# Kernel optimization log

Hardware: AMD Instinct MI355X
Metric: run time of the kernel (lower is better)

## Reference

```python
import jax, jax.numpy as jnp
import numpy as np

B, C, H, W = 8, 512, 128, 128
WS = 8

def _proj(x, w, b):
    # 1x1 conv == channel GEMM: (B,C,H,W) x (Cout,Cin) -> (B,Cout,H,W)
    return jnp.einsum('bchw,oc->bohw', x, w) + b[None, :, None, None]

def _split_windows(x):
    # (B,C,H,W) -> (B*nH*nW, ws*ws, C)
    b, c, h, w = x.shape
    x = x.reshape(b, c, h // WS, WS, w // WS, WS)
    x = x.transpose(0, 2, 4, 3, 5, 1)
    return x.reshape(-1, WS * WS, c)

def _merge_windows(x, b, c, h, w):
    # (B*nH*nW, ws*ws, C) -> (B,C,H,W)
    x = x.reshape(b, h // WS, w // WS, WS, WS, c)
    x = x.transpose(0, 5, 1, 3, 2, 4)
    return x.reshape(b, c, h, w)

def setup_inputs() -> dict:
    key = jax.random.key(0)
    ks = jax.random.split(key, 9)
    s = 1.0 / np.sqrt(C)
    return {
        'x': jax.random.normal(ks[0], (B, C, H, W), jnp.float32),
        'wq': jax.random.normal(ks[1], (C, C), jnp.float32) * s,
        'bq': jnp.zeros((C,), jnp.float32),
        'wk': jax.random.normal(ks[2], (C, C), jnp.float32) * s,
        'bk': jnp.zeros((C,), jnp.float32),
        'wv': jax.random.normal(ks[3], (C, C), jnp.float32) * s,
        'bv': jnp.zeros((C,), jnp.float32),
        'wo': jax.random.normal(ks[4], (C, C), jnp.float32) * s,
        'bo': jnp.zeros((C,), jnp.float32),
    }

def reference(x, wq, bq, wk, bk, wv, bv, wo, bo):
    b, c, h, w = x.shape
    q = _split_windows(_proj(x, wq, bq))  # (nWin, ws*ws, C)
    k = _split_windows(_proj(x, wk, bk))
    v = _split_windows(_proj(x, wv, bv))
    attn = jnp.einsum('nqc,nkc->nqk', q, k) / jnp.sqrt(jnp.asarray(c, x.dtype))
    attn = jax.nn.softmax(attn, axis=-1)
    out = jnp.einsum('nqk,nkc->nqc', attn, v)
    out = _merge_windows(out, b, c, h, w)
    return _proj(out, wo, bo)
```

## Files before the change

kernel.cpp:

```cpp
#include <hip/hip_runtime.h>

typedef __attribute__((ext_vector_type(8))) short bf16x8;
typedef __attribute__((ext_vector_type(4))) float f32x4;

#define MFMA16(a, b, c) __builtin_amdgcn_mfma_f32_16x16x32_bf16((a), (b), (c), 0, 0, 0)

__device__ __forceinline__ float b2f(unsigned short u) {
  unsigned int v = ((unsigned int)u) << 16;
  return __builtin_bit_cast(float, v);
}
__device__ __forceinline__ unsigned short f2b(float f) {
  unsigned int u = __builtin_bit_cast(unsigned int, f);
  u += 0x7fffu + ((u >> 16) & 1u);
  return (unsigned short)(u >> 16);
}
__device__ __forceinline__ void gload16(const void* g, void* l) {
  __builtin_amdgcn_global_load_lds(
      (const __attribute__((address_space(1))) unsigned int*)g,
      (__attribute__((address_space(3))) unsigned int*)l, 16, 0, 0);
}

__global__ __launch_bounds__(256) void k_wprep(
    const float* __restrict__ wq, const float* __restrict__ wk,
    const float* __restrict__ wv, const float* __restrict__ wo,
    unsigned short* __restrict__ outbase) {
  const int z = blockIdx.z;
  const int t = threadIdx.x;
  if (z == 3) {
    const int r0 = blockIdx.x << 6, s0 = blockIdx.y << 6;
    const int row = r0 + (t >> 2), col = s0 + (t & 3) * 16;
    const float* src = wo + (size_t)row * 512 + col;
    unsigned short* dst = outbase + 786432 + (size_t)row * 512 + col;
    unsigned short o[16];
#pragma unroll
    for (int i = 0; i < 4; ++i) {
      const float4 v = ((const float4*)src)[i];
      o[i * 4 + 0] = f2b(v.x); o[i * 4 + 1] = f2b(v.y);
      o[i * 4 + 2] = f2b(v.z); o[i * 4 + 3] = f2b(v.w);
    }
    *(uint4*)dst = *(const uint4*)&o[0];
    *(uint4*)(dst + 8) = *(const uint4*)&o[8];
    return;
  }
  __shared__ unsigned short tile[64][72];
  const float* in = (z == 0) ? wq : (z == 1) ? wk : wv;
  unsigned short* out = outbase + (size_t)z * 262144u;
  const int r0 = blockIdx.x << 6, s0 = blockIdx.y << 6;
  {
    const int sl = t >> 3, rl = (t & 7) << 3;
#pragma unroll
    for (int pass = 0; pass < 2; ++pass) {
      const int s = sl + pass * 32;
      const float* src = in + (size_t)(s0 + s) * 512 + r0 + rl;
      const float4 f0 = ((const float4*)src)[0];
      const float4 f1 = ((const float4*)src)[1];
      tile[rl + 0][s] = f2b(f0.x);
      tile[rl + 1][s] = f2b(f0.y);
      tile[rl + 2][s] = f2b(f0.z);
      tile[rl + 3][s] = f2b(f0.w);
      tile[rl + 4][s] = f2b(f1.x);
      tile[rl + 5][s] = f2b(f1.y);
      tile[rl + 6][s] = f2b(f1.z);
      tile[rl + 7][s] = f2b(f1.w);
    }
  }
  __syncthreads();
  {
    const int rl = t >> 3, sl = (t & 7) << 3;
#pragma unroll
    for (int pass = 0; pass < 2; ++pass) {
      const int r = rl + pass * 32;
      uint4 v = *(const uint4*)&tile[r][sl];
      *(uint4*)(out + (size_t)(r0 + r) * 512 + s0 + sl) = v;
    }
  }
}

__global__ __launch_bounds__(256) void k_bias(
    const float* __restrict__ wo, const float* __restrict__ bv,
    const float* __restrict__ bo, const float* __restrict__ wk,
    const float* __restrict__ bq, float* __restrict__ bvo,
    float* __restrict__ u) {
  const int bid = blockIdx.x;
  if (bid < 2) {
    const int o = bid * 256 + threadIdx.x;
    float acc = bo[o];
    const float* row = wo + (size_t)o * 512;
    for (int j = 0; j < 512; ++j) acc += row[j] * bv[j];
    bvo[o] = acc;
  } else {
    const int c = (bid - 2) * 256 + threadIdx.x;
    float acc = 0.f;
    for (int o = 0; o < 512; ++o) acc += bq[o] * wk[(size_t)o * 512 + c];
    u[c] = acc;
  }
}

__global__ __launch_bounds__(256, 2) void k_transpose(
    const float* __restrict__ X, unsigned short* __restrict__ XT,
    unsigned short* __restrict__ XV) {
  const int hz = blockIdx.x;
  const int c0 = blockIdx.y << 5;
  const int b = blockIdx.z;
  const int h0 = hz << 2;
  const int t = threadIdx.x;
  const int cg = t >> 6, hh = (t >> 4) & 3, wl = t & 15;
  const int c8 = c0 + cg * 8;
  const int h = h0 + hh;

  const float* xsrc = X + (size_t)b * 8388608u + (size_t)c8 * 16384 +
                      (size_t)h * 128 + wl * 8;
  float4 a0[8], a1[8];
#pragma unroll
  for (int ci = 0; ci < 8; ++ci) {
    a0[ci] = ((const float4*)(xsrc + (size_t)ci * 16384))[0];
    a1[ci] = ((const float4*)(xsrc + (size_t)ci * 16384))[1];
  }
  __builtin_amdgcn_sched_barrier(0);

  unsigned short s8[8][8];
#pragma unroll
  for (int ci = 0; ci < 8; ++ci) {
    s8[ci][0] = f2b(a0[ci].x); s8[ci][1] = f2b(a0[ci].y);
    s8[ci][2] = f2b(a0[ci].z); s8[ci][3] = f2b(a0[ci].w);
    s8[ci][4] = f2b(a1[ci].x); s8[ci][5] = f2b(a1[ci].y);
    s8[ci][6] = f2b(a1[ci].z); s8[ci][7] = f2b(a1[ci].w);
  }

  const int win = b * 256 + (h0 >> 3) * 16 + wl;
  const int hrow = h & 7;
  unsigned short* xvdst =
      XV + (size_t)c8 * 131072 + (size_t)win * 64 + hrow * 8;
#pragma unroll
  for (int ci = 0; ci < 8; ++ci)
    *(uint4*)(xvdst + (size_t)ci * 131072) = *(const uint4*)s8[ci];

  unsigned short* xtdst =
      XT + (size_t)b * 8388608u + ((size_t)h * 128 + wl * 8) * 512 + c8;
#pragma unroll
  for (int pi = 0; pi < 8; ++pi) {
    unsigned short o[8];
#pragma unroll
    for (int ci = 0; ci < 8; ++ci) o[ci] = s8[ci][pi];
    *(uint4*)(xtdst + (size_t)pi * 512) = *(const uint4*)o;
  }
}

template <int MODE>
__global__ __launch_bounds__(512, 2) void k_gemm256(
    const unsigned short* __restrict__ A, const unsigned short* __restrict__ B,
    const float* __restrict__ bias0, void* __restrict__ C0v) {
  __shared__ unsigned short lsA[4][256 * 32];
  __shared__ unsigned short lsB[4][256 * 32];
  const int bid = blockIdx.x;
  int mt, nt, sel = 0;
  if (MODE == 0) {
    const int work = ((bid & 7) << 7) + (bid >> 3);
    mt = work >> 1; nt = work & 1;
  } else if (MODE == 2) {
    const int work = ((bid & 7) << 7) + (bid >> 3);
    nt = work >> 1; mt = work & 1;
  } else {
    sel = bid >> 2;
    mt = bid & 1; nt = (bid >> 1) & 1;
  }
  const unsigned short* Ap = A;
  const unsigned short* Bp = B;
  if (MODE == 4) {
    Ap = sel ? A + 786432 : A + 262144;
    Bp = sel ? A + 524288 : A;
  }
  const int m0 = mt << 8, n0 = nt << 8;

  const int t = threadIdx.x;
  const int l = t & 63;
  const int lr = l & 15, lg = l >> 4;
  const int w = t >> 6;
  const int wr = w >> 2, wc = w & 3;
  const int ra = wr << 7, rb = wc << 6;
  const int srowS = t >> 2;
  const int scolS = (t & 3) << 3;
  const int ssw = ((srowS >> 1) & 3) << 3;
  const int scolX = scolS ^ ssw;
  const int rsw = (lr >> 1) & 3;
  const int rco = (lg ^ rsw) * 8;

  f32x4 acc[8][4];
#pragma unroll
  for (int i = 0; i < 8; ++i)
#pragma unroll
    for (int j = 0; j < 4; ++j) acc[i][j] = f32x4{0.f, 0.f, 0.f, 0.f};

  auto stage = [&](int kt) {
    const int buf = kt & 3, k0 = kt << 5;
#pragma unroll
    for (int hh = 0; hh < 2; ++hh) {
      gload16(Ap + (size_t)(m0 + srowS + hh * 128) * 512 + k0 + scolX,
              &lsA[buf][(srowS + hh * 128) * 32 + scolS]);
      gload16(Bp + (size_t)(n0 + srowS + hh * 128) * 512 + k0 + scolX,
              &lsB[buf][(srowS + hh * 128) * 32 + scolS]);
    }
  };
  auto compute = [&](int kt) {
    const int buf = kt & 3;
    bf16x8 af[8], bfv[4];
#pragma unroll
    for (int i = 0; i < 8; ++i)
      af[i] = *(const bf16x8*)&lsA[buf][(ra + i * 16 + lr) * 32 + rco];
#pragma unroll
    for (int j = 0; j < 4; ++j)
      bfv[j] = *(const bf16x8*)&lsB[buf][(rb + j * 16 + lr) * 32 + rco];
    __builtin_amdgcn_s_setprio(1);
#pragma unroll
    for (int i = 0; i < 8; ++i)
#pragma unroll
      for (int j = 0; j < 4; ++j)
        acc[i][j] = MFMA16(af[i], bfv[j], acc[i][j]);
    __builtin_amdgcn_s_setprio(0);
  };

  stage(0); stage(1); stage(2);

#define GITER(kt, vm)                                        \
  asm volatile("s_waitcnt vmcnt(" #vm ")" ::: "memory");     \
  __builtin_amdgcn_s_barrier();                              \
  __builtin_amdgcn_sched_barrier(0);                         \
  if ((kt) + 3 < 16) stage((kt) + 3);                        \
  compute(kt);                                               \
  __builtin_amdgcn_sched_barrier(0);                         \
  __builtin_amdgcn_s_barrier();

  GITER(0, 8)  GITER(1, 8)  GITER(2, 8)  GITER(3, 8)
  GITER(4, 8)  GITER(5, 8)  GITER(6, 8)  GITER(7, 8)
  GITER(8, 8)  GITER(9, 8)  GITER(10, 8) GITER(11, 8)
  GITER(12, 8) GITER(13, 8) GITER(14, 4) GITER(15, 0)
#undef GITER

#pragma unroll
  for (int i = 0; i < 8; ++i) {
    const int cmb = m0 + ra + i * 16 + lg * 4;
#pragma unroll
    for (int j = 0; j < 4; ++j) {
      const int cn = n0 + rb + j * 16 + lr;
      const float bn = (MODE == 0) ? bias0[cn] : 0.f;
#pragma unroll
      for (int r = 0; r < 4; ++r) {
        const int cm = cmb + r;
        if (MODE == 0) {
          ((unsigned short*)C0v)[(size_t)cm * 512 + cn] = f2b(acc[i][j][r] + bn);
        } else if (MODE == 2) {
          const float val = acc[i][j][r] + bias0[cm];
          const int bb = cn >> 14, p = cn & 16383;
          __builtin_nontemporal_store(
              val, (float*)C0v + (size_t)bb * 8388608 + (size_t)cm * 16384 + p);
        } else {
          unsigned short* Cs =
              (unsigned short*)C0v + (sel ? 1048576 : 1572864);
          Cs[(size_t)cm * 512 + cn] = f2b(acc[i][j][r]);
        }
      }
    }
  }
}

__global__ __launch_bounds__(256) void k_attn(
    const unsigned short* __restrict__ Q, const unsigned short* __restrict__ XT,
    const unsigned short* __restrict__ XV, unsigned short* __restrict__ Y) {
  __shared__ unsigned short P_lds[4][64][72];
  const int t = threadIdx.x, w = t >> 6, l = t & 63;
  const int lr = l & 15, lg = l >> 4;
  const int grp = ((blockIdx.x & 7) << 6) + (blockIdx.x >> 3);
  const int win = grp * 4 + w;
  const int b = win >> 8, th = (win >> 4) & 15, tw = win & 15;
  const size_t p_base = (size_t)b * 16384 + (size_t)th * 1024 + (size_t)tw * 8;
  const size_t rowpix = p_base + (size_t)(lr >> 3) * 128 + (lr & 7);
  const unsigned short* qbase = Q + rowpix * 512;
  const unsigned short* kbase = XT + rowpix * 512;

  f32x4 acc[4][4];
#pragma unroll
  for (int i = 0; i < 4; ++i)
#pragma unroll
    for (int j = 0; j < 4; ++j) acc[i][j] = f32x4{0.f, 0.f, 0.f, 0.f};

  bf16x8 kp[2][4], qp[2][4];
#pragma unroll
  for (int pp = 0; pp < 2; ++pp) {
    const int co = pp * 32 + lg * 8;
#pragma unroll
    for (int i = 0; i < 4; ++i) {
      kp[pp][i] = *(const bf16x8*)(kbase + (size_t)i * 131072 + co);
      qp[pp][i] = *(const bf16x8*)(qbase + (size_t)i * 131072 + co);
    }
  }
#pragma unroll
  for (int cs = 0; cs < 16; ++cs) {
    const int cb = cs & 1;
    __builtin_amdgcn_s_setprio(1);
#pragma unroll
    for (int mt = 0; mt < 4; ++mt)
#pragma unroll
      for (int qt = 0; qt < 4; ++qt)
        acc[mt][qt] = MFMA16(kp[cb][mt], qp[cb][qt], acc[mt][qt]);
    __builtin_amdgcn_s_setprio(0);
    if (cs + 2 < 16) {
      const int co = (cs + 2) * 32 + lg * 8;
#pragma unroll
      for (int i = 0; i < 4; ++i) {
        kp[cb][i] = *(const bf16x8*)(kbase + (size_t)i * 131072 + co);
        qp[cb][i] = *(const bf16x8*)(qbase + (size_t)i * 131072 + co);
      }
    }
  }

  const float scale = 0.044194173824159216f;
#pragma unroll
  for (int qt = 0; qt < 4; ++qt) {
    float pv[4][4];
    float mx = -3.0e38f;
#pragma unroll
    for (int mt = 0; mt < 4; ++mt)
#pragma unroll
      for (int j = 0; j < 4; ++j) {
        const float s = acc[mt][qt][j] * scale;
        pv[mt][j] = s;
        mx = fmaxf(mx, s);
      }
    mx = fmaxf(mx, __shfl_xor(mx, 16));
    mx = fmaxf(mx, __shfl_xor(mx, 32));
    float sum = 0.f;
#pragma unroll
    for (int mt = 0; mt < 4; ++mt)
#pragma unroll
      for (int j = 0; j < 4; ++j) {
        const float e = __expf(pv[mt][j] - mx);
        pv[mt][j] = e;
        sum += e;
      }
    sum += __shfl_xor(sum, 16);
    sum += __shfl_xor(sum, 32);
    const float inv = 1.f / sum;
#pragma unroll
    for (int mt = 0; mt < 4; ++mt)
#pragma unroll
      for (int j = 0; j < 4; j += 2) {
        const unsigned int pk =
            (unsigned int)f2b(pv[mt][j] * inv) |
            ((unsigned int)f2b(pv[mt][j + 1] * inv) << 16);
        *(unsigned int*)&P_lds[w][qt * 16 + lr][mt * 16 + lg * 4 + j] = pk;
      }
  }

  bf16x8 pa0[4], pa1[4];
#pragma unroll
  for (int qt = 0; qt < 4; ++qt) {
    pa0[qt] = *(const bf16x8*)&P_lds[w][qt * 16 + lr][lg * 8];
    pa1[qt] = *(const bf16x8*)&P_lds[w][qt * 16 + lr][32 + lg * 8];
  }
  const unsigned short* vbase =
      XV + (size_t)lr * 131072 + (size_t)win * 64 + lg * 8;
  unsigned short* ystore =
      Y + (p_base + (size_t)(lg >> 1) * 128 + ((lg & 1) << 2)) * 512 + lr;

  bf16x8 v0p[2], v1p[2];
#pragma unroll
  for (int pp = 0; pp < 2; ++pp) {
    const unsigned short* vp = vbase + (size_t)pp * (16 * 131072);
    v0p[pp] = *(const bf16x8*)vp;
    v1p[pp] = *(const bf16x8*)(vp + 32);
  }
#pragma unroll
  for (int nt = 0; nt < 32; ++nt) {
    const int cb = nt & 1;
    f32x4 o[4];
    __builtin_amdgcn_s_setprio(1);
#pragma unroll
    for (int qt = 0; qt < 4; ++qt) {
      o[qt] = f32x4{0.f, 0.f, 0.f, 0.f};
      o[qt] = MFMA16(pa0[qt], v0p[cb], o[qt]);
      o[qt] = MFMA16(pa1[qt], v1p[cb], o[qt]);
    }
    __builtin_amdgcn_s_setprio(0);
    if (nt + 2 < 32) {
      const unsigned short* vp = vbase + (size_t)(nt + 2) * (16 * 131072);
      v0p[cb] = *(const bf16x8*)vp;
      v1p[cb] = *(const bf16x8*)(vp + 32);
    }
#pragma unroll
    for (int qt = 0; qt < 4; ++qt)
#pragma unroll
      for (int r = 0; r < 4; ++r)
        ystore[(size_t)qt * 131072 + r * 512 + nt * 16] = f2b(o[qt][r]);
  }
}

extern "C" void kernel_launch(void* const* d_in, const int* in_sizes, int n_in,
                              void* d_out, int out_size, void* d_ws,
                              size_t ws_size, hipStream_t stream) {
  (void)in_sizes; (void)n_in; (void)out_size;
  const float* x = (const float*)d_in[0];
  const float* wq = (const float*)d_in[1];
  const float* bq = (const float*)d_in[2];
  const float* wk = (const float*)d_in[3];
  const float* bk = (const float*)d_in[4];
  const float* wv = (const float*)d_in[5];
  const float* bv = (const float*)d_in[6];
  const float* wo = (const float*)d_in[7];
  const float* bo = (const float*)d_in[8];
  (void)bk;

  const size_t NEED = (size_t)(2097152 + 3 * 67108864) * 2;
  if (ws_size < NEED) return;

  unsigned short* wb = (unsigned short*)d_ws;
  unsigned short* wvo = wb + 1048576;
  float* bvo = (float*)(wb + 1310720);
  float* ub = (float*)(wb + 1311744);
  unsigned short* Bqk = wb + 1572864;
  unsigned short* xT = wb + 2097152;
  unsigned short* xV = xT + 67108864;
  unsigned short* Ybuf = xV + 67108864;
  unsigned short* Tq = (unsigned short*)d_out;

  k_wprep<<<dim3(8, 8, 4), 256, 0, stream>>>(wq, wk, wv, wo, wb);
  k_bias<<<4, 256, 0, stream>>>(wo, bv, bo, wk, bq, bvo, ub);
  k_gemm256<4><<<8, 512, 0, stream>>>(wb, wb, nullptr, wb);
  k_transpose<<<dim3(32, 16, 8), 256, 0, stream>>>(x, xT, xV);
  k_gemm256<0><<<1024, 512, 0, stream>>>(xT, Bqk, ub, Tq);
  k_attn<<<512, 256, 0, stream>>>(Tq, xT, xV, Ybuf);
  k_gemm256<2><<<1024, 512, 0, stream>>>(wvo, Ybuf, bvo, d_out);
}
```

Before: 526.1 us.

## Stage transpose input through double-buffered LDS with async global-to-LDS loads

Rewrites the fp32-to-bf16 transpose/window-split kernel so each block handles 128 channels in 8 stages of 16. Each stage is loaded into a double-buffered LDS tile with global_load_lds, overlapping the next stage's load with conversion and stores of the current one. Writes to XT become 32-byte contiguous chunks of 16 channels, and writes to XV become 64-byte window runs. In exchange it uses 64 KB of LDS per block, launches a quarter as many blocks, and adds barriers that may lower occupancy.

```diff
diff --git a/kernel.cpp b/kernel.cpp
--- a/kernel.cpp
+++ b/kernel.cpp
@@ -99,50 +99,75 @@
 __global__ __launch_bounds__(256, 2) void k_transpose(
     const float* __restrict__ X, unsigned short* __restrict__ XT,
     unsigned short* __restrict__ XV) {
+  __shared__ float lds[2][16 * 512];
   const int hz = blockIdx.x;
-  const int c0 = blockIdx.y << 5;
+  const int cg = blockIdx.y;
   const int b = blockIdx.z;
   const int h0 = hz << 2;
+  const int c0 = cg << 7;
   const int t = threadIdx.x;
-  const int cg = t >> 6, hh = (t >> 4) & 3, wl = t & 15;
-  const int c8 = c0 + cg * 8;
-  const int h = h0 + hh;
-
-  const float* xsrc = X + (size_t)b * 8388608u + (size_t)c8 * 16384 +
-                      (size_t)h * 128 + wl * 8;
-  float4 a0[8], a1[8];
-#pragma unroll
-  for (int ci = 0; ci < 8; ++ci) {
-    a0[ci] = ((const float4*)(xsrc + (size_t)ci * 16384))[0];
-    a1[ci] = ((const float4*)(xsrc + (size_t)ci * 16384))[1];
-  }
-  __builtin_amdgcn_sched_barrier(0);
-
-  unsigned short s8[8][8];
-#pragma unroll
-  for (int ci = 0; ci < 8; ++ci) {
-    s8[ci][0] = f2b(a0[ci].x); s8[ci][1] = f2b(a0[ci].y);
-    s8[ci][2] = f2b(a0[ci].z); s8[ci][3] = f2b(a0[ci].w);
-    s8[ci][4] = f2b(a1[ci].x); s8[ci][5] = f2b(a1[ci].y);
-    s8[ci][6] = f2b(a1[ci].z); s8[ci][7] = f2b(a1[ci].w);
-  }
-
-  const int win = b * 256 + (h0 >> 3) * 16 + wl;
-  const int hrow = h & 7;
-  unsigned short* xvdst =
-      XV + (size_t)c8 * 131072 + (size_t)win * 64 + hrow * 8;
-#pragma unroll
-  for (int ci = 0; ci < 8; ++ci)
-    *(uint4*)(xvdst + (size_t)ci * 131072) = *(const uint4*)s8[ci];
-
-  unsigned short* xtdst =
-      XT + (size_t)b * 8388608u + ((size_t)h * 128 + wl * 8) * 512 + c8;
-#pragma unroll
-  for (int pi = 0; pi < 8; ++pi) {
-    unsigned short o[8];
-#pragma unroll
-    for (int ci = 0; ci < 8; ++ci) o[ci] = s8[ci][pi];
-    *(uint4*)(xtdst + (size_t)pi * 512) = *(const uint4*)o;
+  const float* xb = X + (size_t)b * 8388608u + (size_t)c0 * 16384 +
+                    (size_t)h0 * 128;
+
+  auto stage = [&](int s) {
+    float* dstb = lds[s & 1];
+#pragma unroll
+    for (int i = 0; i < 8; ++i) {
+      const int cl = i * 2 + (t >> 7);
+      const int q = (i * 256 + t) & 127;
+      gload16(xb + (size_t)(s * 16 + cl) * 16384 + q * 4,
+              dstb + (size_t)(i * 256 + t) * 4);
+    }
+  };
+
+  auto consume = [&](int s) {
+    const float* L = lds[s & 1];
+#pragma unroll
+    for (int pp = 0; pp < 2; ++pp) {
+      const int p = t + pp * 256;
+      unsigned short o[16];
+#pragma unroll
+      for (int cl = 0; cl < 16; ++cl) o[cl] = f2b(L[cl * 512 + p]);
+      unsigned short* d =
+          XT + ((size_t)b * 16384 + h0 * 128 + p) * 512 + c0 + s * 16;
+      *(uint4*)d = *(const uint4*)&o[0];
+      *(uint4*)(d + 8) = *(const uint4*)&o[8];
+    }
+    {
+      const int cl = t >> 4, win = t & 15;
+      unsigned short ov[32];
+#pragma unroll
+      for (int hr = 0; hr < 4; ++hr) {
+        const float4 f0 = *(const float4*)&L[cl * 512 + hr * 128 + win * 8];
+        const float4 f1 = *(const float4*)&L[cl * 512 + hr * 128 + win * 8 + 4];
+        ov[hr * 8 + 0] = f2b(f0.x); ov[hr * 8 + 1] = f2b(f0.y);
+        ov[hr * 8 + 2] = f2b(f0.z); ov[hr * 8 + 3] = f2b(f0.w);
+        ov[hr * 8 + 4] = f2b(f1.x); ov[hr * 8 + 5] = f2b(f1.y);
+        ov[hr * 8 + 6] = f2b(f1.z); ov[hr * 8 + 7] = f2b(f1.w);
+      }
+      const int wing = b * 256 + (h0 >> 3) * 16 + win;
+      const int tok0 = (h0 & 4) * 8;
+      unsigned short* dv = XV + (size_t)(c0 + s * 16 + cl) * 131072 +
+                           (size_t)wing * 64 + tok0;
+      *(uint4*)(dv + 0) = *(const uint4*)&ov[0];
+      *(uint4*)(dv + 8) = *(const uint4*)&ov[8];
+      *(uint4*)(dv + 16) = *(const uint4*)&ov[16];
+      *(uint4*)(dv + 24) = *(const uint4*)&ov[24];
+    }
+  };
+
+  stage(0);
+#pragma unroll
+  for (int s = 0; s < 8; ++s) {
+    if (s < 7) {
+      stage(s + 1);
+      asm volatile("s_waitcnt vmcnt(8)" ::: "memory");
+    } else {
+      asm volatile("s_waitcnt vmcnt(0)" ::: "memory");
+    }
+    __builtin_amdgcn_s_barrier();
+    consume(s);
+    __builtin_amdgcn_s_barrier();
   }
 }
 
@@ -425,7 +450,7 @@
   k_wprep<<<dim3(8, 8, 4), 256, 0, stream>>>(wq, wk, wv, wo, wb);
   k_bias<<<4, 256, 0, stream>>>(wo, bv, bo, wk, bq, bvo, ub);
   k_gemm256<4><<<8, 512, 0, stream>>>(wb, wb, nullptr, wb);
-  k_transpose<<<dim3(32, 16, 8), 256, 0, stream>>>(x, xT, xV);
+  k_transpose<<<dim3(32, 4, 8), 256, 0, stream>>>(x, xT, xV);
   k_gemm256<0><<<1024, 512, 0, stream>>>(xT, Bqk, ub, Tq);
   k_attn<<<512, 256, 0, stream>>>(Tq, xT, xV, Ybuf);
   k_gemm256<2><<<1024, 512, 0, stream>>>(wvo, Ybuf, bvo, d_out);
```

Measured after the change: 580.1 us. +10.3%, slower.
